# Kernel optimization log

Measured on AMD Instinct MI355X. Metric: run time of the kernel, lower is better.

## Reference

```python
import jax, jax.numpy as jnp
import numpy as np

T, B, IN_D, HID, OUT_D = 1024, 64, 128, 512, 128


def setup_inputs() -> dict:
    key = jax.random.key(0)
    ks = jax.random.split(key, 8)
    s_ih = 1.0 / np.sqrt(HID)
    return {
        "x": jax.random.normal(ks[0], (T, B, IN_D), dtype=jnp.float32),
        "h0": jax.random.normal(ks[1], (1, B, HID), dtype=jnp.float32),
        "W_ih": jax.random.uniform(ks[2], (HID, IN_D), jnp.float32, -s_ih, s_ih),
        "W_hh": jax.random.uniform(ks[3], (HID, HID), jnp.float32, -s_ih, s_ih),
        "b_ih": jax.random.uniform(ks[4], (HID,), jnp.float32, -s_ih, s_ih),
        "b_hh": jax.random.uniform(ks[5], (HID,), jnp.float32, -s_ih, s_ih),
        "W_fc": jax.random.uniform(ks[6], (OUT_D, HID), jnp.float32, -s_ih, s_ih),
        "b_fc": jax.random.uniform(ks[7], (OUT_D,), jnp.float32, -s_ih, s_ih),
    }


def reference(x, h0, W_ih, W_hh, b_ih, b_hh, W_fc, b_fc):
    # Precompute input projection for all time steps in one big GEMM: [T,B,H]
    xp = jnp.einsum("tbi,hi->tbh", x, W_ih) + b_ih + b_hh

    def step(h, xp_t):
        # Elman cell: h_t = tanh(W_ih x_t + b_ih + W_hh h_{t-1} + b_hh)
        h_new = jnp.tanh(xp_t + h @ W_hh.T)
        return h_new, h_new

    h_last, r = jax.lax.scan(step, h0[0], xp)  # r: [T,B,H]
    y = jnp.einsum("tbh,oh->tbo", r, W_fc) + b_fc  # [T,B,OUT_D]
    return (y, h_last[None, :, :])
```

## Files before the change

### kernel.cpp

```cpp
#include <hip/hip_runtime.h>
#include <hip/hip_bf16.h>
#include <math.h>

#define TT 1024
#define BB 64
#define IND 128
#define HID 512
#define OUTD 128


#define WIH4_OFF 0
#define WFC4_OFF 65536
#define XP_OFF   131072
#define R_OFF    33685504
#define HBUF_OFF 50462720
#define CNT_OFF  50528256

__device__ __forceinline__ float bf2f(unsigned short u) {
    union { unsigned int i; float f; } v; v.i = ((unsigned int)u) << 16; return v.f;
}
__device__ __forceinline__ unsigned short f2bf(float f) {
    union { unsigned int i; float f; } v; v.f = f;
    unsigned int i = v.i;
    unsigned int r = (i + 0x7FFFu + ((i >> 16) & 1u)) >> 16;
    return (unsigned short)r;
}

__global__ void k_prep(const float* __restrict__ wih, const float* __restrict__ wfc,
                       float* __restrict__ ws) {
    int fid = blockIdx.x * 256 + threadIdx.x;
    if (fid < 16384) {
        int k4 = fid >> 9, j = fid & 511;
        ((float4*)(ws + WIH4_OFF))[fid] = ((const float4*)wih)[j * 32 + k4];
    } else if (fid < 32768) {
        int f = fid - 16384;
        int h4 = f >> 7, o = f & 127;
        ((float4*)(ws + WFC4_OFF))[f] = ((const float4*)wfc)[o * 128 + h4];
    }
}

__global__ __launch_bounds__(512) void k_xp(const float* __restrict__ x,
                                            const float* __restrict__ wih4,
                                            const float* __restrict__ bih,
                                            const float* __restrict__ bhh,
                                            float* __restrict__ xp) {
    int t = blockIdx.x, bg = blockIdx.y;
    int j = threadIdx.x;
    __shared__ float4 xs[16 * 32];
    const float4* xsrc = (const float4*)(x + ((size_t)t * BB + bg * 16) * IND);
    xs[j] = xsrc[j];
    __syncthreads();

    float bias = bih[j] + bhh[j];
    float acc[16];
#pragma unroll
    for (int b = 0; b < 16; b++) acc[b] = bias;

    const float4* wp = (const float4*)wih4;
#pragma unroll 4
    for (int k4 = 0; k4 < 32; k4++) {
        float4 w = wp[k4 * 512 + j];
#pragma unroll
        for (int b = 0; b < 16; b++) {
            float4 xv = xs[b * 32 + k4];
            acc[b] += w.x * xv.x + w.y * xv.y + w.z * xv.z + w.w * xv.w;
        }
    }
    float* dst = xp + ((size_t)t * BB + bg * 16) * HID + j;
#pragma unroll
    for (int b = 0; b < 16; b++) dst[(size_t)b * HID] = acc[b];
}

__global__ __launch_bounds__(512, 2) void k_rnn(const float* __restrict__ xp,
                                                const float* __restrict__ whh,
                                                unsigned short* __restrict__ r,
                                                float* __restrict__ out,
                                                float* __restrict__ hbuf,
                                                unsigned int* __restrict__ cnt) {
    const int b = blockIdx.x & 63;
    const int g = blockIdx.x >> 6;
    const int tid = threadIdx.x;
    const int kt = tid >> 5;
    const int jg = tid & 31;
    const int jbase = g * 128;

    float4 wreg[4][8];
    const float4* wsrc = (const float4*)whh;
#pragma unroll
    for (int j4 = 0; j4 < 4; j4++)
#pragma unroll
        for (int i4 = 0; i4 < 8; i4++)
            wreg[j4][i4] = wsrc[(size_t)(jbase + jg * 4 + j4) * 128 + kt * 8 + i4];

    __shared__ float4 hs4[128];
    __shared__ float pbuf[16][128];

    {
        float v = __hip_atomic_load(hbuf + (size_t)b * HID + tid,
                                    __ATOMIC_RELAXED, __HIP_MEMORY_SCOPE_AGENT);
        ((float*)hs4)[tid] = v;
    }
    __syncthreads();

    const float* xpb = xp + (size_t)b * HID + jbase;
    unsigned short* rb = r + (size_t)b * HID + jbase;
    unsigned int* cb = cnt + b * 32;

    float xpv = (tid < 128) ? xpb[tid] : 0.f;
    float hn = 0.f;

    for (int t = 0; t < TT; t++) {
        float4 a0 = {0,0,0,0}, a1 = {0,0,0,0}, a2 = {0,0,0,0}, a3 = {0,0,0,0};
#pragma unroll
        for (int i4 = 0; i4 < 8; i4++) {
            float4 hv = hs4[kt * 8 + i4];
            a0.x += wreg[0][i4].x * hv.x; a0.y += wreg[0][i4].y * hv.y;
            a0.z += wreg[0][i4].z * hv.z; a0.w += wreg[0][i4].w * hv.w;
            a1.x += wreg[1][i4].x * hv.x; a1.y += wreg[1][i4].y * hv.y;
            a1.z += wreg[1][i4].z * hv.z; a1.w += wreg[1][i4].w * hv.w;
            a2.x += wreg[2][i4].x * hv.x; a2.y += wreg[2][i4].y * hv.y;
            a2.z += wreg[2][i4].z * hv.z; a2.w += wreg[2][i4].w * hv.w;
            a3.x += wreg[3][i4].x * hv.x; a3.y += wreg[3][i4].y * hv.y;
            a3.z += wreg[3][i4].z * hv.z; a3.w += wreg[3][i4].w * hv.w;
        }
        *(float4*)&pbuf[kt][jg * 4] = make_float4(
            (a0.x + a0.y) + (a0.z + a0.w), (a1.x + a1.y) + (a1.z + a1.w),
            (a2.x + a2.y) + (a2.z + a2.w), (a3.x + a3.y) + (a3.z + a3.w));
        __syncthreads();

        const int par1 = (t + 1) & 1;
        if (tid < 128) {
            float s = xpv;
#pragma unroll
            for (int k2 = 0; k2 < 16; k2++) s += pbuf[k2][tid];
            hn = tanhf(s);
            rb[(size_t)t * BB * HID + tid] = f2bf(hn);
            __hip_atomic_store(hbuf + (size_t)par1 * BB * HID + (size_t)b * HID + jbase + tid,
                               hn, __ATOMIC_RELAXED, __HIP_MEMORY_SCOPE_AGENT);
        }
        __syncthreads();

        if (tid < 128 && t + 1 < TT) xpv = xpb[(size_t)(t + 1) * BB * HID + tid];

        if (tid == 0) {
            __hip_atomic_fetch_add(cb, 1u, __ATOMIC_RELEASE, __HIP_MEMORY_SCOPE_AGENT);
            unsigned int target = 4u * (unsigned)(t + 1);
            long polls = 0;
            long lim = (t == 0) ? (1L << 22) : (1L << 17);
            while (__hip_atomic_load(cb, __ATOMIC_ACQUIRE, __HIP_MEMORY_SCOPE_AGENT) < target) {
                if (++polls > lim) break;
            }
        }
        __syncthreads();

        {
            float v = __hip_atomic_load(hbuf + (size_t)par1 * BB * HID + (size_t)b * HID + tid,
                                        __ATOMIC_RELAXED, __HIP_MEMORY_SCOPE_AGENT);
            ((float*)hs4)[tid] = v;
        }
        __syncthreads();
    }

    if (tid < 128)
        out[(size_t)TT * BB * OUTD + (size_t)b * HID + jbase + tid] = hn;
}

__global__ __launch_bounds__(512) void k_y(const unsigned short* __restrict__ r,
                                           const float* __restrict__ wfc4,
                                           const float* __restrict__ bfc,
                                           float* __restrict__ y) {
    int t = blockIdx.x, bg = blockIdx.y;
    int tid = threadIdx.x;
    int o = tid & 127, bq = tid >> 7;
    __shared__ float rs[16 * 512];
    const unsigned short* rsrc = r + ((size_t)t * BB + bg * 16) * HID;
    for (int i = tid; i < 16 * 512 / 2; i += 512) {
        ushort2 u = ((const ushort2*)rsrc)[i];
        rs[2 * i] = bf2f(u.x);
        rs[2 * i + 1] = bf2f(u.y);
    }
    __syncthreads();

    float acc[4] = {0.f, 0.f, 0.f, 0.f};
    const float4* wp = (const float4*)wfc4;
    const float4* rs4 = (const float4*)rs;
#pragma unroll 4
    for (int h4 = 0; h4 < 128; h4++) {
        float4 w = wp[h4 * 128 + o];
#pragma unroll
        for (int bb = 0; bb < 4; bb++) {
            float4 rv = rs4[(bq * 4 + bb) * 128 + h4];
            acc[bb] += w.x * rv.x + w.y * rv.y + w.z * rv.z + w.w * rv.w;
        }
    }
    float bias = bfc[o];
    float* dst = y + ((size_t)t * BB + bg * 16 + bq * 4) * OUTD + o;
#pragma unroll
    for (int bb = 0; bb < 4; bb++) dst[(size_t)bb * OUTD] = acc[bb] + bias;
}

extern "C" void kernel_launch(void* const* d_in, const int* in_sizes, int n_in,
                              void* d_out, int out_size, void* d_ws, size_t ws_size,
                              hipStream_t stream) {
    (void)in_sizes; (void)n_in; (void)out_size; (void)ws_size;
    const float* x    = (const float*)d_in[0];
    const float* h0   = (const float*)d_in[1];
    const float* wih  = (const float*)d_in[2];
    const float* whh  = (const float*)d_in[3];
    const float* bih  = (const float*)d_in[4];
    const float* bhh  = (const float*)d_in[5];
    const float* wfc  = (const float*)d_in[6];
    const float* bfc  = (const float*)d_in[7];
    float* out = (float*)d_out;

    float* ws = (float*)d_ws;
    float* wih4 = ws + WIH4_OFF;
    float* wfc4 = ws + WFC4_OFF;
    float* xp   = ws + XP_OFF;
    unsigned short* rbuf = (unsigned short*)(ws + R_OFF);
    float* hbuf = ws + HBUF_OFF;
    unsigned int* cnt = (unsigned int*)(ws + CNT_OFF);

    hipMemsetAsync(cnt, 0, 64 * 32 * sizeof(unsigned int), stream);
    hipMemcpyAsync(hbuf, h0, (size_t)BB * HID * sizeof(float),
                   hipMemcpyDeviceToDevice, stream);
    hipLaunchKernelGGL(k_prep, dim3(128), dim3(256), 0, stream, wih, wfc, ws);
    hipLaunchKernelGGL(k_xp, dim3(TT, BB / 16), dim3(512), 0, stream, x, wih4, bih, bhh, xp);
    hipLaunchKernelGGL(k_rnn, dim3(256), dim3(512), 0, stream, xp, whh, rbuf, out, hbuf, cnt);
    hipLaunchKernelGGL(k_y, dim3(TT, BB / 16), dim3(512), 0, stream, rbuf, wfc4, bfc, out);
}
```

Baseline: 6.082 ms.

## Restructure recurrent matvec to 4 threads per row with shuffle reduction

```diff
diff --git a/kernel.cpp b/kernel.cpp
--- a/kernel.cpp
+++ b/kernel.cpp
@@ -80,67 +80,59 @@
     const int b = blockIdx.x & 63;
     const int g = blockIdx.x >> 6;
     const int tid = threadIdx.x;
-    const int kt = tid >> 5;
-    const int jg = tid & 31;
-    const int jbase = g * 128;
-
-    float4 wreg[4][8];
-    const float4* wsrc = (const float4*)whh;
-#pragma unroll
-    for (int j4 = 0; j4 < 4; j4++)
-#pragma unroll
-        for (int i4 = 0; i4 < 8; i4++)
-            wreg[j4][i4] = wsrc[(size_t)(jbase + jg * 4 + j4) * 128 + kt * 8 + i4];
-
-    __shared__ float4 hs4[128];
-    __shared__ float pbuf[16][128];
-
+    const int j = tid >> 2;
+    const int q = tid & 3;
+    const int row = g * 128 + j;
+
+    float w[128];
     {
-        float v = __hip_atomic_load(hbuf + (size_t)b * HID + tid,
-                                    __ATOMIC_RELAXED, __HIP_MEMORY_SCOPE_AGENT);
-        ((float*)hs4)[tid] = v;
-    }
+        const float4* wsrc = (const float4*)(whh + (size_t)row * HID + q * 128);
+#pragma unroll
+        for (int i = 0; i < 32; i++) {
+            float4 v = wsrc[i];
+            w[4 * i] = v.x; w[4 * i + 1] = v.y; w[4 * i + 2] = v.z; w[4 * i + 3] = v.w;
+        }
+    }
+#pragma unroll
+    for (int i = 0; i < 128; i++) asm volatile("" : "+v"(w[i]));
+
+    __shared__ float hs[528];
+    hs[tid + 4 * (tid >> 7)] =
+        __hip_atomic_load(hbuf + (size_t)b * HID + tid,
+                          __ATOMIC_RELAXED, __HIP_MEMORY_SCOPE_AGENT);
     __syncthreads();
 
-    const float* xpb = xp + (size_t)b * HID + jbase;
-    unsigned short* rb = r + (size_t)b * HID + jbase;
+    const float* xpb = xp + (size_t)b * HID + row;
+    unsigned short* rb = r + (size_t)b * HID + row;
     unsigned int* cb = cnt + b * 32;
 
-    float xpv = (tid < 128) ? xpb[tid] : 0.f;
+    float xpv = xpb[0];
     float hn = 0.f;
 
     for (int t = 0; t < TT; t++) {
-        float4 a0 = {0,0,0,0}, a1 = {0,0,0,0}, a2 = {0,0,0,0}, a3 = {0,0,0,0};
-#pragma unroll
-        for (int i4 = 0; i4 < 8; i4++) {
-            float4 hv = hs4[kt * 8 + i4];
-            a0.x += wreg[0][i4].x * hv.x; a0.y += wreg[0][i4].y * hv.y;
-            a0.z += wreg[0][i4].z * hv.z; a0.w += wreg[0][i4].w * hv.w;
-            a1.x += wreg[1][i4].x * hv.x; a1.y += wreg[1][i4].y * hv.y;
-            a1.z += wreg[1][i4].z * hv.z; a1.w += wreg[1][i4].w * hv.w;
-            a2.x += wreg[2][i4].x * hv.x; a2.y += wreg[2][i4].y * hv.y;
-            a2.z += wreg[2][i4].z * hv.z; a2.w += wreg[2][i4].w * hv.w;
-            a3.x += wreg[3][i4].x * hv.x; a3.y += wreg[3][i4].y * hv.y;
-            a3.z += wreg[3][i4].z * hv.z; a3.w += wreg[3][i4].w * hv.w;
-        }
-        *(float4*)&pbuf[kt][jg * 4] = make_float4(
-            (a0.x + a0.y) + (a0.z + a0.w), (a1.x + a1.y) + (a1.z + a1.w),
-            (a2.x + a2.y) + (a2.z + a2.w), (a3.x + a3.y) + (a3.z + a3.w));
+        const float4* h4 = (const float4*)(hs + q * 132);
+        float a0 = 0.f, a1 = 0.f, a2 = 0.f, a3 = 0.f;
+#pragma unroll
+        for (int i = 0; i < 32; i++) {
+            float4 hv = h4[i];
+            a0 += w[4 * i + 0] * hv.x;
+            a1 += w[4 * i + 1] * hv.y;
+            a2 += w[4 * i + 2] * hv.z;
+            a3 += w[4 * i + 3] * hv.w;
+        }
+        float s = (a0 + a1) + (a2 + a3);
+        s += __shfl_xor(s, 1, 64);
+        s += __shfl_xor(s, 2, 64);
+        hn = tanhf(s + xpv);
+
+        const int par1 = (t + 1) & 1;
+        if (q == 0) {
+            __hip_atomic_store(hbuf + (size_t)par1 * (BB * HID) + (size_t)b * HID + row,
+                               hn, __ATOMIC_RELAXED, __HIP_MEMORY_SCOPE_AGENT);
+            rb[(size_t)t * BB * HID] = f2bf(hn);
+        }
+        float xpn = (t + 1 < TT) ? xpb[(size_t)(t + 1) * BB * HID] : 0.f;
         __syncthreads();
-
-        const int par1 = (t + 1) & 1;
-        if (tid < 128) {
-            float s = xpv;
-#pragma unroll
-            for (int k2 = 0; k2 < 16; k2++) s += pbuf[k2][tid];
-            hn = tanhf(s);
-            rb[(size_t)t * BB * HID + tid] = f2bf(hn);
-            __hip_atomic_store(hbuf + (size_t)par1 * BB * HID + (size_t)b * HID + jbase + tid,
-                               hn, __ATOMIC_RELAXED, __HIP_MEMORY_SCOPE_AGENT);
-        }
-        __syncthreads();
-
-        if (tid < 128 && t + 1 < TT) xpv = xpb[(size_t)(t + 1) * BB * HID + tid];
 
         if (tid == 0) {
             __hip_atomic_fetch_add(cb, 1u, __ATOMIC_RELEASE, __HIP_MEMORY_SCOPE_AGENT);
@@ -153,16 +145,15 @@
         }
         __syncthreads();
 
-        {
-            float v = __hip_atomic_load(hbuf + (size_t)par1 * BB * HID + (size_t)b * HID + tid,
-                                        __ATOMIC_RELAXED, __HIP_MEMORY_SCOPE_AGENT);
-            ((float*)hs4)[tid] = v;
-        }
+        hs[tid + 4 * (tid >> 7)] =
+            __hip_atomic_load(hbuf + (size_t)par1 * (BB * HID) + (size_t)b * HID + tid,
+                              __ATOMIC_RELAXED, __HIP_MEMORY_SCOPE_AGENT);
+        xpv = xpn;
         __syncthreads();
     }
 
-    if (tid < 128)
-        out[(size_t)TT * BB * OUTD + (size_t)b * HID + jbase + tid] = hn;
+    if (q == 0)
+        out[(size_t)TT * BB * OUTD + (size_t)b * HID + row] = hn;
 }
 
 __global__ __launch_bounds__(512) void k_y(const unsigned short* __restrict__ r,
```

Result: slower. 7.265 ms (+19.5%).
